# Optimization experiments

Hardware: AMD Instinct MI355X
Metric: run time of the kernel (lower is better)

The kernel has to match this reference:

```python
import jax, jax.numpy as jnp
import numpy as np


def setup_inputs() -> dict:
    key = jax.random.key(0)
    k1, k2 = jax.random.split(key)
    video_feat = jax.random.normal(k1, (64, 1024, 512), dtype=jnp.float32)
    lang_feat = jax.random.normal(k2, (64, 512, 512), dtype=jnp.float32)
    return {"video_feat": video_feat, "lang_feat": lang_feat}


def _batch_pairwise_dist(x, y):
    # x: [B, Nv, D], y: [B, Nl, D] -> [B, Nv, Nl] squared-L2 (expanded form)
    a = jnp.sum(x * x, axis=2, keepdims=True)            # [B, Nv, 1]
    b = jnp.sum(y * y, axis=2, keepdims=True)            # [B, Nl, 1]
    ab = jnp.einsum('bvd,bld->bvl', x, y)                # [B, Nv, Nl]
    return a - 2.0 * ab + jnp.swapaxes(b, 1, 2)


def reference(video_feat, lang_feat):
    pairwise_dist = _batch_pairwise_dist(video_feat, lang_feat)  # [B, Nv, Nl]
    Nv = pairwise_dist.shape[1]
    Nl = pairwise_dist.shape[2]
    language_to_clip_dist = jnp.min(pairwise_dist, axis=2).sum(axis=1) / Nv
    clip_to_language_dist = jnp.min(pairwise_dist, axis=1).sum(axis=1) / Nl
    return language_to_clip_dist + clip_to_language_dist  # [B]
```

## Files before the change

### kernel.cpp

```cpp
#include <hip/hip_runtime.h>
#include <math.h>

#define BATCH 64
#define NV 1024
#define NL 512
#define DIM 512
#define TMM 128
#define TNN 128
#define BK 32
#define NKT (DIM / BK)

typedef __bf16 bf16x8 __attribute__((ext_vector_type(8)));
typedef __bf16 bf16x4 __attribute__((ext_vector_type(4)));
typedef float f32x4 __attribute__((ext_vector_type(4)));

__global__ __launch_bounds__(256, 2) void fused_distmin_kernel(
    const float* __restrict__ video, const float* __restrict__ lang,
    float* __restrict__ rowpart, float* __restrict__ colpart) {
    __shared__ __align__(16) ushort AsU[2][4][TMM][8];
    __shared__ __align__(16) ushort BsU[2][4][TNN][8];
    __shared__ float anrm[TMM], bnrm[TNN];
    __shared__ float rowred[2][TMM], colred[2][TNN];

    const int wg = ((blockIdx.x & 7) << 8) | (blockIdx.x >> 3);
    const int b = wg >> 5;
    const int r5 = wg & 31;
    const int mt = r5 >> 2;
    const int nt = r5 & 3;

    const int tid = threadIdx.x;
    const int lane = tid & 63;
    const int w = tid >> 6;
    const int wrow = w >> 1;
    const int wcol = w & 1;
    const int lr = lane & 15;
    const int g = lane >> 4;

    const int srow = tid >> 3;
    const int skq = tid & 7;
    const int o_sl = skq >> 1;
    const int half = skq & 1;

    const float* Ath = video + ((size_t)b * NV + (size_t)mt * TMM + srow) * DIM + skq * 4;
    const float* Bth = lang + ((size_t)b * NL + (size_t)nt * TNN + srow) * DIM + skq * 4;

    float nA[4] = {0.f, 0.f, 0.f, 0.f};
    float nB[4] = {0.f, 0.f, 0.f, 0.f};

    f32x4 acc[4][4];
#pragma unroll
    for (int i = 0; i < 4; i++)
#pragma unroll
        for (int j = 0; j < 4; j++) acc[i][j] = (f32x4){0.f, 0.f, 0.f, 0.f};

    float4 va[4], vb[4];

    auto load_chunk = [&](int k0) {
#pragma unroll
        for (int t = 0; t < 4; ++t) {
            va[t] = *(const float4*)(Ath + (size_t)t * 32 * DIM + k0);
            vb[t] = *(const float4*)(Bth + (size_t)t * 32 * DIM + k0);
        }
    };
    auto write_chunk = [&](int buf) {
#pragma unroll
        for (int t = 0; t < 4; ++t) {
            float4 v = va[t];
            nA[t] += v.x * v.x + v.y * v.y + v.z * v.z + v.w * v.w;
            bf16x4 p = {(__bf16)v.x, (__bf16)v.y, (__bf16)v.z, (__bf16)v.w};
            *(bf16x4*)&AsU[buf][o_sl][srow + 32 * t][half * 4] = p;
            float4 u = vb[t];
            nB[t] += u.x * u.x + u.y * u.y + u.z * u.z + u.w * u.w;
            bf16x4 q = {(__bf16)u.x, (__bf16)u.y, (__bf16)u.z, (__bf16)u.w};
            *(bf16x4*)&BsU[buf][o_sl][srow + 32 * t][half * 4] = q;
        }
    };

    load_chunk(0);
    write_chunk(0);
    __syncthreads();

    for (int kt = 0; kt < NKT; ++kt) {
        const int cur = kt & 1;
        const bool more = (kt + 1) < NKT;
        if (more) load_chunk((kt + 1) * BK);

        bf16x8 av[4], bv[4];
#pragma unroll
        for (int fr = 0; fr < 4; ++fr)
            av[fr] = *(const bf16x8*)&AsU[cur][g][wrow * 64 + fr * 16 + lr][0];
#pragma unroll
        for (int fc = 0; fc < 4; ++fc)
            bv[fc] = *(const bf16x8*)&BsU[cur][g][wcol * 64 + fc * 16 + lr][0];
#pragma unroll
        for (int fr = 0; fr < 4; ++fr)
#pragma unroll
            for (int fc = 0; fc < 4; ++fc)
                acc[fr][fc] = __builtin_amdgcn_mfma_f32_16x16x32_bf16(
                    av[fr], bv[fc], acc[fr][fc], 0, 0, 0);

        if (more) write_chunk(cur ^ 1);
        __syncthreads();
    }

#pragma unroll
    for (int t = 0; t < 4; ++t) {
#pragma unroll
        for (int s = 1; s < 8; s <<= 1) {
            nA[t] += __shfl_xor(nA[t], s);
            nB[t] += __shfl_xor(nB[t], s);
        }
    }
    if ((tid & 7) == 0) {
#pragma unroll
        for (int t = 0; t < 4; ++t) {
            anrm[srow + 32 * t] = nA[t];
            bnrm[srow + 32 * t] = nB[t];
        }
    }
    __syncthreads();

    const int rgrp = (lane >> 4) * 4;
    float anorm[4][4];
#pragma unroll
    for (int fr = 0; fr < 4; ++fr)
#pragma unroll
        for (int r = 0; r < 4; ++r)
            anorm[fr][r] = anrm[wrow * 64 + fr * 16 + rgrp + r];
    float bnorm[4];
#pragma unroll
    for (int fc = 0; fc < 4; ++fc)
        bnorm[fc] = bnrm[wcol * 64 + fc * 16 + lr];

    float rmin[4][4];
    float cmin[4];
#pragma unroll
    for (int fr = 0; fr < 4; ++fr)
#pragma unroll
        for (int r = 0; r < 4; ++r) rmin[fr][r] = INFINITY;
#pragma unroll
    for (int fc = 0; fc < 4; ++fc) cmin[fc] = INFINITY;

#pragma unroll
    for (int fr = 0; fr < 4; ++fr)
#pragma unroll
        for (int fc = 0; fc < 4; ++fc)
#pragma unroll
            for (int r = 0; r < 4; ++r) {
                float d = anorm[fr][r] - 2.0f * acc[fr][fc][r] + bnorm[fc];
                rmin[fr][r] = fminf(rmin[fr][r], d);
                cmin[fc] = fminf(cmin[fc], d);
            }

#pragma unroll
    for (int fr = 0; fr < 4; ++fr)
#pragma unroll
        for (int r = 0; r < 4; ++r) {
#pragma unroll
            for (int off = 1; off < 16; off <<= 1)
                rmin[fr][r] = fminf(rmin[fr][r], __shfl_xor(rmin[fr][r], off));
        }
#pragma unroll
    for (int fc = 0; fc < 4; ++fc) {
#pragma unroll
        for (int off = 16; off < 64; off <<= 1)
            cmin[fc] = fminf(cmin[fc], __shfl_xor(cmin[fc], off));
    }

    if ((lane & 15) == 0) {
#pragma unroll
        for (int fr = 0; fr < 4; ++fr)
#pragma unroll
            for (int r = 0; r < 4; ++r)
                rowred[wcol][wrow * 64 + fr * 16 + rgrp + r] = rmin[fr][r];
    }
    if (lane < 16) {
#pragma unroll
        for (int fc = 0; fc < 4; ++fc)
            colred[wrow][wcol * 64 + fc * 16 + lane] = cmin[fc];
    }
    __syncthreads();
    if (tid < TMM) {
        rowpart[((size_t)(b * 4 + nt)) * NV + mt * TMM + tid] =
            fminf(rowred[0][tid], rowred[1][tid]);
    } else {
        int c2 = tid - TMM;
        colpart[((size_t)(b * 8 + mt)) * NL + nt * TNN + c2] =
            fminf(colred[0][c2], colred[1][c2]);
    }
}

__global__ __launch_bounds__(256) void reduce2_kernel(
    const float* __restrict__ rowpart, const float* __restrict__ colpart,
    float* __restrict__ out) {
    int b = blockIdx.x;
    int tid = threadIdx.x;
    float s = 0.0f;
    for (int r = tid; r < NV; r += 256) {
        float m = INFINITY;
#pragma unroll
        for (int nt = 0; nt < 4; nt++)
            m = fminf(m, rowpart[((size_t)(b * 4 + nt)) * NV + r]);
        s += m * (1.0f / NV);
    }
    for (int c = tid; c < NL; c += 256) {
        float m = INFINITY;
#pragma unroll
        for (int mt = 0; mt < 8; mt++)
            m = fminf(m, colpart[((size_t)(b * 8 + mt)) * NL + c]);
        s += m * (1.0f / NL);
    }
    __shared__ float red[4];
#pragma unroll
    for (int off = 32; off > 0; off >>= 1) s += __shfl_down(s, off);
    if ((tid & 63) == 0) red[tid >> 6] = s;
    __syncthreads();
    if (tid == 0) out[b] = red[0] + red[1] + red[2] + red[3];
}

extern "C" void kernel_launch(void* const* d_in, const int* in_sizes, int n_in,
                              void* d_out, int out_size, void* d_ws, size_t ws_size,
                              hipStream_t stream) {
    const float* video = (const float*)d_in[0];
    const float* lang = (const float*)d_in[1];
    float* out = (float*)d_out;

    float* rowpart = (float*)d_ws;
    float* colpart = rowpart + (size_t)BATCH * 4 * NV;

    fused_distmin_kernel<<<dim3(2048), 256, 0, stream>>>(video, lang, rowpart, colpart);
    reduce2_kernel<<<BATCH, 256, 0, stream>>>(rowpart, colpart, out);
}
```

Baseline: 78.32 us.

## Double register prefetch two K-chunks ahead with lighter barriers and higher occupancy

The K loop is unrolled by two and uses two register sets, so global loads for chunk k+2 are issued while chunk k is multiplied, giving each load more time in flight. The plain __syncthreads is replaced by a barrier that waits only on LDS and scalar memory counters (lgkmcnt), so outstanding global loads are not drained at each barrier. Launch bounds are raised to 3 blocks per CU to allow more resident waves. The extra prefetch registers together with the tighter register budget from the higher occupancy target could cause spills.

```diff
diff --git a/kernel.cpp b/kernel.cpp
--- a/kernel.cpp
+++ b/kernel.cpp
@@ -14,7 +14,12 @@
 typedef __bf16 bf16x4 __attribute__((ext_vector_type(4)));
 typedef float f32x4 __attribute__((ext_vector_type(4)));
 
-__global__ __launch_bounds__(256, 2) void fused_distmin_kernel(
+#define BARRIER() do { \
+    asm volatile("s_waitcnt lgkmcnt(0)" ::: "memory"); \
+    __builtin_amdgcn_s_barrier(); \
+} while (0)
+
+__global__ __launch_bounds__(256, 3) void fused_distmin_kernel(
     const float* __restrict__ video, const float* __restrict__ lang,
     float* __restrict__ rowpart, float* __restrict__ colpart) {
     __shared__ __align__(16) ushort AsU[2][4][TMM][8];
@@ -53,55 +58,63 @@
 #pragma unroll
         for (int j = 0; j < 4; j++) acc[i][j] = (f32x4){0.f, 0.f, 0.f, 0.f};
 
-    float4 va[4], vb[4];
-
-    auto load_chunk = [&](int k0) {
-#pragma unroll
-        for (int t = 0; t < 4; ++t) {
-            va[t] = *(const float4*)(Ath + (size_t)t * 32 * DIM + k0);
-            vb[t] = *(const float4*)(Bth + (size_t)t * 32 * DIM + k0);
-        }
-    };
-    auto write_chunk = [&](int buf) {
-#pragma unroll
-        for (int t = 0; t < 4; ++t) {
-            float4 v = va[t];
-            nA[t] += v.x * v.x + v.y * v.y + v.z * v.z + v.w * v.w;
-            bf16x4 p = {(__bf16)v.x, (__bf16)v.y, (__bf16)v.z, (__bf16)v.w};
-            *(bf16x4*)&AsU[buf][o_sl][srow + 32 * t][half * 4] = p;
-            float4 u = vb[t];
-            nB[t] += u.x * u.x + u.y * u.y + u.z * u.z + u.w * u.w;
-            bf16x4 q = {(__bf16)u.x, (__bf16)u.y, (__bf16)u.z, (__bf16)u.w};
-            *(bf16x4*)&BsU[buf][o_sl][srow + 32 * t][half * 4] = q;
-        }
-    };
-
-    load_chunk(0);
-    write_chunk(0);
-    __syncthreads();
-
-    for (int kt = 0; kt < NKT; ++kt) {
-        const int cur = kt & 1;
-        const bool more = (kt + 1) < NKT;
-        if (more) load_chunk((kt + 1) * BK);
-
-        bf16x8 av[4], bv[4];
-#pragma unroll
-        for (int fr = 0; fr < 4; ++fr)
-            av[fr] = *(const bf16x8*)&AsU[cur][g][wrow * 64 + fr * 16 + lr][0];
-#pragma unroll
-        for (int fc = 0; fc < 4; ++fc)
-            bv[fc] = *(const bf16x8*)&BsU[cur][g][wcol * 64 + fc * 16 + lr][0];
-#pragma unroll
-        for (int fr = 0; fr < 4; ++fr)
-#pragma unroll
-            for (int fc = 0; fc < 4; ++fc)
-                acc[fr][fc] = __builtin_amdgcn_mfma_f32_16x16x32_bf16(
-                    av[fr], bv[fc], acc[fr][fc], 0, 0, 0);
-
-        if (more) write_chunk(cur ^ 1);
-        __syncthreads();
-    }
+    float4 va0[4], vb0[4], va1[4], vb1[4];
+
+#define LOADSET(S, K0)                                                         \
+    {                                                                          \
+        _Pragma("unroll") for (int t = 0; t < 4; ++t) {                        \
+            va##S[t] = *(const float4*)(Ath + (size_t)t * 32 * DIM + (K0));    \
+            vb##S[t] = *(const float4*)(Bth + (size_t)t * 32 * DIM + (K0));    \
+        }                                                                      \
+    }
+
+#define WRITESET(S)                                                            \
+    {                                                                          \
+        _Pragma("unroll") for (int t = 0; t < 4; ++t) {                        \
+            float4 v = va##S[t];                                               \
+            nA[t] += v.x * v.x + v.y * v.y + v.z * v.z + v.w * v.w;            \
+            bf16x4 p = {(__bf16)v.x, (__bf16)v.y, (__bf16)v.z, (__bf16)v.w};   \
+            *(bf16x4*)&AsU[S][o_sl][srow + 32 * t][half * 4] = p;              \
+            float4 u = vb##S[t];                                               \
+            nB[t] += u.x * u.x + u.y * u.y + u.z * u.z + u.w * u.w;            \
+            bf16x4 q = {(__bf16)u.x, (__bf16)u.y, (__bf16)u.z, (__bf16)u.w};   \
+            *(bf16x4*)&BsU[S][o_sl][srow + 32 * t][half * 4] = q;              \
+        }                                                                      \
+    }
+
+#define MFMA_PHASE(C)                                                          \
+    {                                                                          \
+        bf16x8 av[4], bv[4];                                                   \
+        _Pragma("unroll") for (int fr = 0; fr < 4; ++fr)                       \
+            av[fr] = *(const bf16x8*)&AsU[C][g][wrow * 64 + fr * 16 + lr][0];  \
+        _Pragma("unroll") for (int fc = 0; fc < 4; ++fc)                       \
+            bv[fc] = *(const bf16x8*)&BsU[C][g][wcol * 64 + fc * 16 + lr][0];  \
+        _Pragma("unroll") for (int fr = 0; fr < 4; ++fr)                       \
+            _Pragma("unroll") for (int fc = 0; fc < 4; ++fc)                   \
+                acc[fr][fc] = __builtin_amdgcn_mfma_f32_16x16x32_bf16(         \
+                    av[fr], bv[fc], acc[fr][fc], 0, 0, 0);                     \
+    }
+
+    LOADSET(0, 0);
+    LOADSET(1, BK);
+    WRITESET(0);
+    BARRIER();
+
+#pragma unroll 1
+    for (int kt = 0; kt < NKT - 2; kt += 2) {
+        LOADSET(0, (kt + 2) * BK);
+        MFMA_PHASE(0);
+        WRITESET(1);
+        BARRIER();
+        LOADSET(1, (kt + 3) * BK);
+        MFMA_PHASE(1);
+        WRITESET(0);
+        BARRIER();
+    }
+    MFMA_PHASE(0);
+    WRITESET(1);
+    BARRIER();
+    MFMA_PHASE(1);
 
 #pragma unroll
     for (int t = 0; t < 4; ++t) {
```

New measurement: 89.15 us. 1.14x slower.

## Enlarge M tile to 256 with 512-thread blocks to reuse B tiles

Applied to the files above, without the earlier changes.

Doubles the video tile to 256 rows per workgroup, with 8 waves arranged 4x2, and halves the grid to 1024 blocks. Each language tile is now loaded once per 256 video rows instead of per 128, which cuts redundant global reads and bf16 conversion of the lang operand. The column-min reduction now combines four wave-rows, and the partial buffers and final reduce use 4 M-tiles instead of 8. The trade-off is larger shared memory and more threads per block, which may lower occupancy, and fewer blocks to spread across the CUs.

```diff
diff --git a/kernel.cpp b/kernel.cpp
--- a/kernel.cpp
+++ b/kernel.cpp
@@ -5,7 +5,7 @@
 #define NV 1024
 #define NL 512
 #define DIM 512
-#define TMM 128
+#define TMM 256
 #define TNN 128
 #define BK 32
 #define NKT (DIM / BK)
@@ -14,19 +14,18 @@
 typedef __bf16 bf16x4 __attribute__((ext_vector_type(4)));
 typedef float f32x4 __attribute__((ext_vector_type(4)));
 
-__global__ __launch_bounds__(256, 2) void fused_distmin_kernel(
+__global__ __launch_bounds__(512, 2) void fused_distmin_kernel(
     const float* __restrict__ video, const float* __restrict__ lang,
     float* __restrict__ rowpart, float* __restrict__ colpart) {
     __shared__ __align__(16) ushort AsU[2][4][TMM][8];
     __shared__ __align__(16) ushort BsU[2][4][TNN][8];
     __shared__ float anrm[TMM], bnrm[TNN];
-    __shared__ float rowred[2][TMM], colred[2][TNN];
-
-    const int wg = ((blockIdx.x & 7) << 8) | (blockIdx.x >> 3);
-    const int b = wg >> 5;
-    const int r5 = wg & 31;
-    const int mt = r5 >> 2;
-    const int nt = r5 & 3;
+    __shared__ float rowred[2][TMM], colred[4][TNN];
+
+    const int wg = ((blockIdx.x & 7) << 7) | (blockIdx.x >> 3);
+    const int b = wg >> 4;
+    const int mt = (wg >> 2) & 3;
+    const int nt = wg & 3;
 
     const int tid = threadIdx.x;
     const int lane = tid & 63;
@@ -45,7 +44,7 @@
     const float* Bth = lang + ((size_t)b * NL + (size_t)nt * TNN + srow) * DIM + skq * 4;
 
     float nA[4] = {0.f, 0.f, 0.f, 0.f};
-    float nB[4] = {0.f, 0.f, 0.f, 0.f};
+    float nB[2] = {0.f, 0.f};
 
     f32x4 acc[4][4];
 #pragma unroll
@@ -53,14 +52,15 @@
 #pragma unroll
         for (int j = 0; j < 4; j++) acc[i][j] = (f32x4){0.f, 0.f, 0.f, 0.f};
 
-    float4 va[4], vb[4];
+    float4 va[4], vb[2];
 
     auto load_chunk = [&](int k0) {
 #pragma unroll
-        for (int t = 0; t < 4; ++t) {
-            va[t] = *(const float4*)(Ath + (size_t)t * 32 * DIM + k0);
-            vb[t] = *(const float4*)(Bth + (size_t)t * 32 * DIM + k0);
-        }
+        for (int t = 0; t < 4; ++t)
+            va[t] = *(const float4*)(Ath + (size_t)t * 64 * DIM + k0);
+#pragma unroll
+        for (int t = 0; t < 2; ++t)
+            vb[t] = *(const float4*)(Bth + (size_t)t * 64 * DIM + k0);
     };
     auto write_chunk = [&](int buf) {
 #pragma unroll
@@ -68,11 +68,14 @@
             float4 v = va[t];
             nA[t] += v.x * v.x + v.y * v.y + v.z * v.z + v.w * v.w;
             bf16x4 p = {(__bf16)v.x, (__bf16)v.y, (__bf16)v.z, (__bf16)v.w};
-            *(bf16x4*)&AsU[buf][o_sl][srow + 32 * t][half * 4] = p;
+            *(bf16x4*)&AsU[buf][o_sl][srow + 64 * t][half * 4] = p;
+        }
+#pragma unroll
+        for (int t = 0; t < 2; ++t) {
             float4 u = vb[t];
             nB[t] += u.x * u.x + u.y * u.y + u.z * u.z + u.w * u.w;
             bf16x4 q = {(__bf16)u.x, (__bf16)u.y, (__bf16)u.z, (__bf16)u.w};
-            *(bf16x4*)&BsU[buf][o_sl][srow + 32 * t][half * 4] = q;
+            *(bf16x4*)&BsU[buf][o_sl][srow + 64 * t][half * 4] = q;
         }
     };
 
@@ -104,19 +107,17 @@
     }
 
 #pragma unroll
-    for (int t = 0; t < 4; ++t) {
-#pragma unroll
-        for (int s = 1; s < 8; s <<= 1) {
-            nA[t] += __shfl_xor(nA[t], s);
-            nB[t] += __shfl_xor(nB[t], s);
-        }
+    for (int s = 1; s < 8; s <<= 1) {
+#pragma unroll
+        for (int t = 0; t < 4; ++t) nA[t] += __shfl_xor(nA[t], s);
+#pragma unroll
+        for (int t = 0; t < 2; ++t) nB[t] += __shfl_xor(nB[t], s);
     }
     if ((tid & 7) == 0) {
 #pragma unroll
-        for (int t = 0; t < 4; ++t) {
-            anrm[srow + 32 * t] = nA[t];
-            bnrm[srow + 32 * t] = nB[t];
-        }
+        for (int t = 0; t < 4; ++t) anrm[srow + 64 * t] = nA[t];
+#pragma unroll
+        for (int t = 0; t < 2; ++t) bnrm[srow + 64 * t] = nB[t];
     }
     __syncthreads();
 
@@ -183,10 +184,11 @@
     if (tid < TMM) {
         rowpart[((size_t)(b * 4 + nt)) * NV + mt * TMM + tid] =
             fminf(rowred[0][tid], rowred[1][tid]);
-    } else {
+    } else if (tid < TMM + TNN) {
         int c2 = tid - TMM;
-        colpart[((size_t)(b * 8 + mt)) * NL + nt * TNN + c2] =
-            fminf(colred[0][c2], colred[1][c2]);
+        colpart[((size_t)(b * 4 + mt)) * NL + nt * TNN + c2] =
+            fminf(fminf(colred[0][c2], colred[1][c2]),
+                  fminf(colred[2][c2], colred[3][c2]));
     }
 }
 
@@ -206,8 +208,8 @@
     for (int c = tid; c < NL; c += 256) {
         float m = INFINITY;
 #pragma unroll
-        for (int mt = 0; mt < 8; mt++)
-            m = fminf(m, colpart[((size_t)(b * 8 + mt)) * NL + c]);
+        for (int mt = 0; mt < 4; mt++)
+            m = fminf(m, colpart[((size_t)(b * 4 + mt)) * NL + c]);
         s += m * (1.0f / NL);
     }
     __shared__ float red[4];
@@ -228,6 +230,6 @@
     float* rowpart = (float*)d_ws;
     float* colpart = rowpart + (size_t)BATCH * 4 * NV;
 
-    fused_distmin_kernel<<<dim3(2048), 256, 0, stream>>>(video, lang, rowpart, colpart);
+    fused_distmin_kernel<<<dim3(1024), 512, 0, stream>>>(video, lang, rowpart, colpart);
     reduce2_kernel<<<BATCH, 256, 0, stream>>>(rowpart, colpart, out);
 }
```

Measured after the change: 69.24 us. 11.6% less time.
